# Kernel optimization log

Measured on AMD Instinct MI355X. Metric: run time of the kernel, lower is better.

The kernel has to match this reference:

```python
import jax, jax.numpy as jnp
import numpy as np

K = 1  # top-k from init_kwargs


def setup_inputs() -> dict:
    key = jax.random.key(0)
    k0, k1, k2, k3, k4, k5 = jax.random.split(key, 6)
    B, L, Ed, NE = 8192, 1024, 1024, 8
    D = L + Ed  # input_dim = latent_dim + embed_dim
    s = 1.0 / np.sqrt(D)  # torch nn.Linear default init bound
    x = jax.random.normal(k0, (B, L), dtype=jnp.float32)
    y = jax.random.normal(k1, (B, Ed), dtype=jnp.float32)
    We = jax.random.uniform(k2, (NE, D, D), dtype=jnp.float32, minval=-s, maxval=s)  # expert weights [E, out, in]
    be = jax.random.uniform(k3, (NE, D), dtype=jnp.float32, minval=-s, maxval=s)
    gW = jax.random.uniform(k4, (NE, D), dtype=jnp.float32, minval=-s, maxval=s)  # gate weight [E, in]
    gb = jax.random.uniform(k5, (NE,), dtype=jnp.float32, minval=-s, maxval=s)
    return {"x": x, "y": y, "We": We, "be": be, "gW": gW, "gb": gb}


def reference(x, y, We, be, gW, gb):
    # inp: [B, D]
    inp = jnp.concatenate([x, y], axis=1)
    # gate logits: [B, E] (eval mode: no noise)
    gate_logits = inp @ gW.T + gb
    topk_val, topk_idx = jax.lax.top_k(gate_logits, K)  # [B, K]
    topk_gates = jax.nn.softmax(topk_val, axis=1)       # [B, K]
    # dense compute-all-experts (faithful to original): [B, E, D]
    all_out = jnp.einsum('bd,eod->beo', inp, We) + be[None, :, :]
    # gather top-k experts per token: [B, K, D]
    gathered = jnp.take_along_axis(all_out, topk_idx[:, :, None], axis=1)
    fused = jnp.sum(gathered * topk_gates[:, :, None], axis=1)  # [B, D]
    return fused
```

## Files before the change

kernel.cpp:

```cpp
#include <hip/hip_runtime.h>
#include <stdint.h>

#define B_TOK 8192
#define DIM   2048
#define NE    8
#define BM 128
#define BN 128
#define BK 64
#define CVT_BLOCKS 8192
#define NT3 32

typedef __bf16 bf16x8 __attribute__((ext_vector_type(8)));
typedef float  f32x4  __attribute__((ext_vector_type(4)));

__device__ __forceinline__ unsigned short f2b(float f) {
  unsigned u = __builtin_bit_cast(unsigned, f);
  u += 0x7fffu + ((u >> 16) & 1u);
  return (unsigned short)(u >> 16);
}
__device__ __forceinline__ uint2 pack4(float4 v) {
  uint2 r;
  r.x = (unsigned)f2b(v.x) | ((unsigned)f2b(v.y) << 16);
  r.y = (unsigned)f2b(v.z) | ((unsigned)f2b(v.w) << 16);
  return r;
}
__device__ __forceinline__ uint2 pack4(f32x4 v) {
  uint2 r;
  r.x = (unsigned)f2b(v.x) | ((unsigned)f2b(v.y) << 16);
  r.y = (unsigned)f2b(v.z) | ((unsigned)f2b(v.w) << 16);
  return r;
}
__device__ __forceinline__ void gload16(const void* g, void* l) {
  __builtin_amdgcn_global_load_lds(
      (const __attribute__((address_space(1))) void*)g,
      (__attribute__((address_space(3))) void*)l, 16, 0, 0);
}

#define SCHEDB __builtin_amdgcn_sched_barrier(0)
#define BARRIER do { SCHEDB; __builtin_amdgcn_s_barrier(); SCHEDB; } while (0)

template <bool WINP>
__global__ __launch_bounds__(256) void gate_kernel(
    const float* __restrict__ x,
    const float* __restrict__ y,
    const float* __restrict__ gW,
    const float* __restrict__ gb,
    int* __restrict__ eid,
    unsigned short* __restrict__ inpB) {
  const int tid = threadIdx.x;
  const int ln = tid & 63;
  const int token = blockIdx.x * 4 + (tid >> 6);

  double acc[NE];
#pragma unroll
  for (int e = 0; e < NE; ++e) acc[e] = 0.0;

  const float* bases[2] = {x, y};
#pragma unroll
  for (int p = 0; p < 2; ++p) {
    const float* rowp = bases[p] + (size_t)token * 1024;
#pragma unroll
    for (int it = 0; it < 4; ++it) {
      const int d = it * 256 + ln * 4;
      float4 v = *(const float4*)(rowp + d);
      if (WINP)
        *(uint2*)(inpB + (size_t)token * DIM + p * 1024 + d) = pack4(v);
#pragma unroll
      for (int e = 0; e < NE; ++e) {
        float4 g = *(const float4*)(gW + e * DIM + p * 1024 + d);
        acc[e] += (double)v.x * (double)g.x + (double)v.y * (double)g.y +
                  (double)v.z * (double)g.z + (double)v.w * (double)g.w;
      }
    }
  }
#pragma unroll
  for (int e = 0; e < NE; ++e) {
#pragma unroll
    for (int off = 32; off >= 1; off >>= 1) acc[e] += __shfl_xor(acc[e], off, 64);
  }
  if (ln == 0) {
    int best = 0;
    double bv = acc[0] + (double)gb[0];
#pragma unroll
    for (int e = 1; e < NE; ++e) {
      double v = acc[e] + (double)gb[e];
      if (v > bv) { bv = v; best = e; }
    }
    eid[token] = best;
  }
}

template <bool CVT>
__global__ __launch_bounds__(256) void bucket_cvt(
    const int* __restrict__ eid,
    int* __restrict__ counts,
    int* __restrict__ perm,
    const float* __restrict__ We,
    unsigned short* __restrict__ WeB) {
  if (CVT && blockIdx.x >= NE) {
    const int cb = blockIdx.x - NE;
    const size_t base = (size_t)cb * 1024;
#pragma unroll
    for (int j = 0; j < 4; ++j) {
      size_t i4 = base + (size_t)(j * 256 + threadIdx.x);
      f32x4 v = __builtin_nontemporal_load((const f32x4*)We + i4);
      *(uint2*)(WeB + i4 * 4) = pack4(v);
    }
    return;
  }

  const int e = blockIdx.x;
  const int tid = threadIdx.x, ln = tid & 63, wv = tid >> 6;
  __shared__ int wsum[4];
  __shared__ int basev;
  if (tid == 0) basev = 0;
  __syncthreads();
  for (int t0 = 0; t0 < B_TOK; t0 += 256) {
    int t = t0 + tid;
    bool m = (eid[t] == e);
    unsigned long long mk = __ballot(m);
    int pre = __popcll(mk & ((1ull << ln) - 1ull));
    if (ln == 0) wsum[wv] = __popcll(mk);
    __syncthreads();
    int off = basev;
    for (int w = 0; w < wv; ++w) off += wsum[w];
    if (m) perm[e * B_TOK + off + pre] = t;
    __syncthreads();
    if (tid == 0) basev += wsum[0] + wsum[1] + wsum[2] + wsum[3];
    __syncthreads();
  }
  if (tid == 0) counts[e] = basev;
}

__global__ __launch_bounds__(512, 2) void moe_gemm4(
    const float* __restrict__ be,
    const unsigned short* __restrict__ inpB,
    const unsigned short* __restrict__ WeB,
    const int* __restrict__ counts,
    const int* __restrict__ perm,
    float* __restrict__ out) {
  __shared__ __align__(16) unsigned short AB[65536];
  __shared__ int tokLds[256];

  const int bid = blockIdx.x;
  const int e = bid & 7;
  const int j = bid >> 3;
  const int n0 = (j & 7) * 256;
  const int m0 = (j >> 3) * 256;
  const int cnt = counts[e];
  if (m0 >= cnt) return;

  const int tid = threadIdx.x;
  const int ln = tid & 63;
  const int wv = tid >> 6;
  const int wm = wv & 1;
  const int wn = wv >> 1;

  if (tid < 256) {
    int r = m0 + tid;
    tokLds[tid] = perm[e * B_TOK + (r < cnt ? r : cnt - 1)];
  }
  __syncthreads();

  const int g = (ln & 7) ^ (ln >> 3);
  const unsigned short* wbbase = WeB + (size_t)e * DIM * DIM;
  const unsigned short* aS[2][2];
  const unsigned short* bS[2][2];
#pragma unroll
  for (int h = 0; h < 2; ++h)
#pragma unroll
    for (int i = 0; i < 2; ++i) {
      int row = h * 128 + (wv * 2 + i) * 8 + (ln >> 3);
      aS[h][i] = inpB + (size_t)tokLds[row] * DIM + g * 8;
      bS[h][i] = wbbase + (size_t)(n0 + row) * DIM + g * 8;
    }

  f32x4 acc[8][4];
#pragma unroll
  for (int a = 0; a < 8; ++a)
#pragma unroll
    for (int b = 0; b < 4; ++b) acc[a][b] = (f32x4){0.f, 0.f, 0.f, 0.f};

  const int aBase = (wm * 128 + (ln & 15)) * 64;
  const int bBase = (wn * 64 + (ln & 15)) * 64;
  const int ofk0 = (((ln >> 4)) ^ (ln & 7)) * 8;
  const int ofk1 = ((4 + (ln >> 4)) ^ (ln & 7)) * 8;

  auto SA = [&](int tt, int h) {
    if (tt >= NT3) return;
    const int dd = (tt & 1) * 16384;
    const int ko = tt * 64;
    gload16(aS[h][0] + ko, &AB[dd + h * 8192 + (wv * 2 + 0) * 512]);
    gload16(aS[h][1] + ko, &AB[dd + h * 8192 + (wv * 2 + 1) * 512]);
  };
  auto SBst = [&](int tt, int h) {
    if (tt >= NT3) return;
    const int dd = (tt & 1) * 16384;
    const int ko = tt * 64;
    gload16(bS[h][0] + ko, &AB[32768 + dd + h * 8192 + (wv * 2 + 0) * 512]);
    gload16(bS[h][1] + ko, &AB[32768 + dd + h * 8192 + (wv * 2 + 1) * 512]);
  };
  auto RAV = [&](bf16x8 (&av)[4][2], int d, int mq) {
#pragma unroll
    for (int f = 0; f < 4; ++f) {
      av[f][0] = *(const bf16x8*)&AB[d + aBase + mq * 4096 + f * 1024 + ofk0];
      av[f][1] = *(const bf16x8*)&AB[d + aBase + mq * 4096 + f * 1024 + ofk1];
    }
  };
  auto RBV = [&](bf16x8 (&bv)[2][2], int d, int nq) {
#pragma unroll
    for (int jj = 0; jj < 2; ++jj) {
      bv[jj][0] = *(const bf16x8*)&AB[32768 + d + bBase + nq * 2048 + jj * 1024 + ofk0];
      bv[jj][1] = *(const bf16x8*)&AB[32768 + d + bBase + nq * 2048 + jj * 1024 + ofk1];
    }
  };
  auto QM = [&](int mq, int nq, bf16x8 (&av)[4][2], bf16x8 (&bv)[2][2]) {
    __builtin_amdgcn_s_setprio(1);
#pragma unroll
    for (int f = 0; f < 4; ++f)
#pragma unroll
      for (int jj = 0; jj < 2; ++jj)
#pragma unroll
        for (int ks = 0; ks < 2; ++ks)
          acc[mq * 4 + f][nq * 2 + jj] = __builtin_amdgcn_mfma_f32_16x16x32_bf16(
              av[f][ks], bv[jj][ks], acc[mq * 4 + f][nq * 2 + jj], 0, 0, 0);
    __builtin_amdgcn_s_setprio(0);
  };

  SA(0, 0); SA(0, 1); SBst(0, 0); SBst(0, 1); SBst(1, 0); SBst(1, 1);
  asm volatile("s_waitcnt vmcnt(4)" ::: "memory");
  BARRIER;

  for (int t = 0; t < NT3; ++t) {
    const int d = (t & 1) * 16384;
    bf16x8 av[4][2], bv0[2][2], bv1[2][2];
    RAV(av, d, 0); RBV(bv0, d, 0);
    SA(t + 1, 0);
    BARRIER;
    QM(0, 0, av, bv0);
    BARRIER;
    RBV(bv1, d, 1);
    SA(t + 1, 1);
    BARRIER;
    QM(0, 1, av, bv1);
    BARRIER;
    RAV(av, d, 1);
    SBst(t + 2, 0);
    BARRIER;
    QM(1, 1, av, bv1);
    BARRIER;
    SBst(t + 2, 1);
    if (t < NT3 - 2) {
      asm volatile("s_waitcnt vmcnt(4)" ::: "memory");
    } else {
      asm volatile("s_waitcnt vmcnt(0)" ::: "memory");
    }
    BARRIER;
    QM(1, 0, av, bv0);
    BARRIER;
  }

  float bias[4]; int col[4];
#pragma unroll
  for (int b = 0; b < 4; ++b) {
    col[b] = n0 + wn * 64 + b * 16 + (ln & 15);
    bias[b] = be[e * DIM + col[b]];
  }
#pragma unroll
  for (int a = 0; a < 8; ++a) {
    int rbase = wm * 128 + a * 16 + ((ln >> 4) << 2);
#pragma unroll
    for (int r = 0; r < 4; ++r) {
      int rl = rbase + r;
      if (m0 + rl < cnt) {
        size_t t = (size_t)tokLds[rl];
#pragma unroll
        for (int b = 0; b < 4; ++b)
          __builtin_nontemporal_store(acc[a][b][r] + bias[b],
                                      &out[t * DIM + col[b]]);
      }
    }
  }
}

__global__ __launch_bounds__(256) void moe_gemm_f32(
    const float* __restrict__ x,
    const float* __restrict__ y,
    const float* __restrict__ We,
    const float* __restrict__ be,
    const int* __restrict__ counts,
    const int* __restrict__ perm,
    float* __restrict__ out) {
  __shared__ unsigned short As[BM * BK];
  __shared__ unsigned short Bs[BN * BK];
  __shared__ int tokLds[BM];

  const int e = blockIdx.z;
  const int cnt = counts[e];
  const int m0 = blockIdx.y * BM;
  if (m0 >= cnt) return;
  const int n0 = blockIdx.x * BN;

  const int tid = threadIdx.x;
  const int ln = tid & 63;
  const int wv = tid >> 6;
  const int wm = wv & 1, wn = wv >> 1;

  if (tid < BM) {
    int r = m0 + tid;
    tokLds[tid] = perm[e * B_TOK + (r < cnt ? r : cnt - 1)];
  }
  __syncthreads();

  const float* wfbase = We + (size_t)e * DIM * DIM;

  f32x4 acc[4][4];
#pragma unroll
  for (int i = 0; i < 4; ++i)
#pragma unroll
    for (int j = 0; j < 4; ++j) acc[i][j] = (f32x4){0.f, 0.f, 0.f, 0.f};

  for (int k0 = 0; k0 < DIM; k0 += BK) {
    __syncthreads();
    const float* ab = (k0 < 1024) ? x : y;
    const int kk = k0 & 1023;
#pragma unroll
    for (int i = 0; i < 8; ++i) {
      int li = i * 256 + tid;
      int row = li >> 4, k4 = li & 15;
      int chunk = k4 >> 1, half = k4 & 1;
      int slot = (chunk ^ (row & 7)) * 2 + half;
      int tok = tokLds[row];
      float4 va = *(const float4*)(ab + (size_t)tok * 1024 + kk + k4 * 4);
      *(uint2*)&As[row * BK + slot * 4] = pack4(va);
      float4 vb = *(const float4*)(wfbase + (size_t)(n0 + row) * DIM + k0 + k4 * 4);
      *(uint2*)&Bs[row * BK + slot * 4] = pack4(vb);
    }
    __syncthreads();

#pragma unroll
    for (int ks = 0; ks < 2; ++ks) {
      bf16x8 av[4], bv[4];
#pragma unroll
      for (int i = 0; i < 4; ++i) {
        int rA = wm * 64 + i * 16 + (ln & 15);
        int c = ks * 4 + (ln >> 4);
        av[i] = *(const bf16x8*)&As[rA * BK + (c ^ (rA & 7)) * 8];
      }
#pragma unroll
      for (int j = 0; j < 4; ++j) {
        int rB = wn * 64 + j * 16 + (ln & 15);
        int c = ks * 4 + (ln >> 4);
        bv[j] = *(const bf16x8*)&Bs[rB * BK + (c ^ (rB & 7)) * 8];
      }
#pragma unroll
      for (int i = 0; i < 4; ++i)
#pragma unroll
        for (int j = 0; j < 4; ++j)
          acc[i][j] = __builtin_amdgcn_mfma_f32_16x16x32_bf16(av[i], bv[j], acc[i][j], 0, 0, 0);
    }
  }

  float bias[4]; int col[4];
#pragma unroll
  for (int j = 0; j < 4; ++j) {
    col[j] = n0 + wn * 64 + j * 16 + (ln & 15);
    bias[j] = be[e * DIM + col[j]];
  }
#pragma unroll
  for (int i = 0; i < 4; ++i) {
    int rbase = wm * 64 + i * 16 + ((ln >> 4) << 2);
#pragma unroll
    for (int r = 0; r < 4; ++r) {
      int rl = rbase + r;
      if (m0 + rl < cnt) {
        size_t t = (size_t)tokLds[rl];
#pragma unroll
        for (int j = 0; j < 4; ++j)
          out[t * DIM + col[j]] = acc[i][j][r] + bias[j];
      }
    }
  }
}

extern "C" void kernel_launch(void* const* d_in, const int* in_sizes, int n_in,
                              void* d_out, int out_size, void* d_ws, size_t ws_size,
                              hipStream_t stream) {
  const float* x  = (const float*)d_in[0];
  const float* y  = (const float*)d_in[1];
  const float* We = (const float*)d_in[2];
  const float* be = (const float*)d_in[3];
  const float* gW = (const float*)d_in[4];
  const float* gb = (const float*)d_in[5];
  float* out = (float*)d_out;

  char* ws = (char*)d_ws;
  int* counts = (int*)ws;
  int* eid    = (int*)(ws + 256);
  int* perm   = (int*)(ws + 33024);
  unsigned short* inpB = (unsigned short*)(ws + 295168);
  unsigned short* WeB  = (unsigned short*)(ws + 33849600);
  const size_t needed = 33849600ull + 67108864ull;

  if (ws_size >= needed) {
    gate_kernel<true><<<dim3(B_TOK / 4), 256, 0, stream>>>(x, y, gW, gb, eid, inpB);
    bucket_cvt<true><<<dim3(NE + CVT_BLOCKS), 256, 0, stream>>>(eid, counts, perm, We, WeB);
    moe_gemm4<<<dim3(2048), 512, 0, stream>>>(be, inpB, WeB, counts, perm, out);
  } else {
    gate_kernel<false><<<dim3(B_TOK / 4), 256, 0, stream>>>(x, y, gW, gb, eid, nullptr);
    bucket_cvt<false><<<dim3(NE), 256, 0, stream>>>(eid, counts, perm, nullptr, nullptr);
    moe_gemm_f32<<<dim3(DIM / BN, B_TOK / BM, NE), 256, 0, stream>>>(
        x, y, We, be, counts, perm, out);
  }
}
```

Measured before the change: 399.6 us.

## Simplify MoE GEMM main loop to BK=32 double-buffered single-phase pipeline

```diff
diff --git a/kernel.cpp b/kernel.cpp
--- a/kernel.cpp
+++ b/kernel.cpp
@@ -8,7 +8,7 @@
 #define BN 128
 #define BK 64
 #define CVT_BLOCKS 8192
-#define NT3 32
+#define NT5 64
 
 typedef __bf16 bf16x8 __attribute__((ext_vector_type(8)));
 typedef float  f32x4  __attribute__((ext_vector_type(4)));
@@ -132,14 +132,14 @@
   if (tid == 0) counts[e] = basev;
 }
 
-__global__ __launch_bounds__(512, 2) void moe_gemm4(
+__global__ __launch_bounds__(512, 2) void moe_gemm5(
     const float* __restrict__ be,
     const unsigned short* __restrict__ inpB,
     const unsigned short* __restrict__ WeB,
     const int* __restrict__ counts,
     const int* __restrict__ perm,
     float* __restrict__ out) {
-  __shared__ __align__(16) unsigned short AB[65536];
+  __shared__ __align__(16) unsigned short AB[32768];
   __shared__ int tokLds[256];
 
   const int bid = blockIdx.x;
@@ -162,18 +162,14 @@
   }
   __syncthreads();
 
-  const int g = (ln & 7) ^ (ln >> 3);
+  const int g = (ln & 3) ^ ((ln >> 3) & 3);
   const unsigned short* wbbase = WeB + (size_t)e * DIM * DIM;
-  const unsigned short* aS[2][2];
-  const unsigned short* bS[2][2];
-#pragma unroll
-  for (int h = 0; h < 2; ++h)
-#pragma unroll
-    for (int i = 0; i < 2; ++i) {
-      int row = h * 128 + (wv * 2 + i) * 8 + (ln >> 3);
-      aS[h][i] = inpB + (size_t)tokLds[row] * DIM + g * 8;
-      bS[h][i] = wbbase + (size_t)(n0 + row) * DIM + g * 8;
-    }
+  const int row0 = 0 * 128 + wv * 16 + (ln >> 2);
+  const int row1 = 1 * 128 + wv * 16 + (ln >> 2);
+  const unsigned short* aS0 = inpB + (size_t)tokLds[row0] * DIM + g * 8;
+  const unsigned short* aS1 = inpB + (size_t)tokLds[row1] * DIM + g * 8;
+  const unsigned short* bS0 = wbbase + (size_t)(n0 + row0) * DIM + g * 8;
+  const unsigned short* bS1 = wbbase + (size_t)(n0 + row1) * DIM + g * 8;
 
   f32x4 acc[8][4];
 #pragma unroll
@@ -181,82 +177,48 @@
 #pragma unroll
     for (int b = 0; b < 4; ++b) acc[a][b] = (f32x4){0.f, 0.f, 0.f, 0.f};
 
-  const int aBase = (wm * 128 + (ln & 15)) * 64;
-  const int bBase = (wn * 64 + (ln & 15)) * 64;
-  const int ofk0 = (((ln >> 4)) ^ (ln & 7)) * 8;
-  const int ofk1 = ((4 + (ln >> 4)) ^ (ln & 7)) * 8;
-
-  auto SA = [&](int tt, int h) {
-    if (tt >= NT3) return;
-    const int dd = (tt & 1) * 16384;
-    const int ko = tt * 64;
-    gload16(aS[h][0] + ko, &AB[dd + h * 8192 + (wv * 2 + 0) * 512]);
-    gload16(aS[h][1] + ko, &AB[dd + h * 8192 + (wv * 2 + 1) * 512]);
+  const int slotR = (ln >> 4) ^ (((ln & 15) >> 1) & 3);
+  const int aOff = (wm * 128 + (ln & 15)) * 32 + slotR * 8;
+  const int bOff = 16384 + (wn * 64 + (ln & 15)) * 32 + slotR * 8;
+
+  auto SA5 = [&](int tt) {
+    if (tt >= NT5) return;
+    const int dd = (tt & 1) * 8192;
+    const int ko = tt * 32;
+    gload16(aS0 + ko, &AB[dd + wv * 512]);
+    gload16(aS1 + ko, &AB[dd + 4096 + wv * 512]);
   };
-  auto SBst = [&](int tt, int h) {
-    if (tt >= NT3) return;
-    const int dd = (tt & 1) * 16384;
-    const int ko = tt * 64;
-    gload16(bS[h][0] + ko, &AB[32768 + dd + h * 8192 + (wv * 2 + 0) * 512]);
-    gload16(bS[h][1] + ko, &AB[32768 + dd + h * 8192 + (wv * 2 + 1) * 512]);
+  auto SB5 = [&](int tt) {
+    if (tt >= NT5) return;
+    const int dd = (tt & 1) * 8192;
+    const int ko = tt * 32;
+    gload16(bS0 + ko, &AB[16384 + dd + wv * 512]);
+    gload16(bS1 + ko, &AB[16384 + dd + 4096 + wv * 512]);
   };
-  auto RAV = [&](bf16x8 (&av)[4][2], int d, int mq) {
-#pragma unroll
-    for (int f = 0; f < 4; ++f) {
-      av[f][0] = *(const bf16x8*)&AB[d + aBase + mq * 4096 + f * 1024 + ofk0];
-      av[f][1] = *(const bf16x8*)&AB[d + aBase + mq * 4096 + f * 1024 + ofk1];
-    }
-  };
-  auto RBV = [&](bf16x8 (&bv)[2][2], int d, int nq) {
-#pragma unroll
-    for (int jj = 0; jj < 2; ++jj) {
-      bv[jj][0] = *(const bf16x8*)&AB[32768 + d + bBase + nq * 2048 + jj * 1024 + ofk0];
-      bv[jj][1] = *(const bf16x8*)&AB[32768 + d + bBase + nq * 2048 + jj * 1024 + ofk1];
-    }
-  };
-  auto QM = [&](int mq, int nq, bf16x8 (&av)[4][2], bf16x8 (&bv)[2][2]) {
+
+  SA5(0); SB5(0);
+  asm volatile("s_waitcnt vmcnt(0)" ::: "memory");
+  BARRIER;
+
+  for (int t = 0; t < NT5; ++t) {
+    const int dd = (t & 1) * 8192;
+    bf16x8 av[8], bv[4];
+#pragma unroll
+    for (int f = 0; f < 8; ++f)
+      av[f] = *(const bf16x8*)&AB[dd + aOff + f * 512];
+#pragma unroll
+    for (int b = 0; b < 4; ++b)
+      bv[b] = *(const bf16x8*)&AB[dd + bOff + b * 512];
+    SA5(t + 1); SB5(t + 1);
+    BARRIER;
     __builtin_amdgcn_s_setprio(1);
 #pragma unroll
-    for (int f = 0; f < 4; ++f)
-#pragma unroll
-      for (int jj = 0; jj < 2; ++jj)
-#pragma unroll
-        for (int ks = 0; ks < 2; ++ks)
-          acc[mq * 4 + f][nq * 2 + jj] = __builtin_amdgcn_mfma_f32_16x16x32_bf16(
-              av[f][ks], bv[jj][ks], acc[mq * 4 + f][nq * 2 + jj], 0, 0, 0);
+    for (int f = 0; f < 8; ++f)
+#pragma unroll
+      for (int b = 0; b < 4; ++b)
+        acc[f][b] = __builtin_amdgcn_mfma_f32_16x16x32_bf16(av[f], bv[b], acc[f][b], 0, 0, 0);
     __builtin_amdgcn_s_setprio(0);
-  };
-
-  SA(0, 0); SA(0, 1); SBst(0, 0); SBst(0, 1); SBst(1, 0); SBst(1, 1);
-  asm volatile("s_waitcnt vmcnt(4)" ::: "memory");
-  BARRIER;
-
-  for (int t = 0; t < NT3; ++t) {
-    const int d = (t & 1) * 16384;
-    bf16x8 av[4][2], bv0[2][2], bv1[2][2];
-    RAV(av, d, 0); RBV(bv0, d, 0);
-    SA(t + 1, 0);
-    BARRIER;
-    QM(0, 0, av, bv0);
-    BARRIER;
-    RBV(bv1, d, 1);
-    SA(t + 1, 1);
-    BARRIER;
-    QM(0, 1, av, bv1);
-    BARRIER;
-    RAV(av, d, 1);
-    SBst(t + 2, 0);
-    BARRIER;
-    QM(1, 1, av, bv1);
-    BARRIER;
-    SBst(t + 2, 1);
-    if (t < NT3 - 2) {
-      asm volatile("s_waitcnt vmcnt(4)" ::: "memory");
-    } else {
-      asm volatile("s_waitcnt vmcnt(0)" ::: "memory");
-    }
-    BARRIER;
-    QM(1, 0, av, bv0);
+    asm volatile("s_waitcnt vmcnt(0)" ::: "memory");
     BARRIER;
   }
 
@@ -405,7 +367,7 @@
   if (ws_size >= needed) {
     gate_kernel<true><<<dim3(B_TOK / 4), 256, 0, stream>>>(x, y, gW, gb, eid, inpB);
     bucket_cvt<true><<<dim3(NE + CVT_BLOCKS), 256, 0, stream>>>(eid, counts, perm, We, WeB);
-    moe_gemm4<<<dim3(2048), 512, 0, stream>>>(be, inpB, WeB, counts, perm, out);
+    moe_gemm5<<<dim3(2048), 512, 0, stream>>>(be, inpB, WeB, counts, perm, out);
   } else {
     gate_kernel<false><<<dim3(B_TOK / 4), 256, 0, stream>>>(x, y, gW, gb, eid, nullptr);
     bucket_cvt<false><<<dim3(NE), 256, 0, stream>>>(eid, counts, perm, nullptr, nullptr);
```

After: 391.5 us. -2.0%, faster.
